# Kernel optimization log

Measured on AMD Instinct MI355X. Metric: run time of the kernel, lower is better.

Reference implementation:

```python
import jax, jax.numpy as jnp
import numpy as np

B, LAT, HID, N, H = 16, 128, 256, 256, 4
C = HID // H
TAU = 1.0


def setup_inputs() -> dict:
    key = jax.random.key(0)
    ks = jax.random.split(key, 16)
    g = lambda k, shape: (jax.random.normal(k, shape, dtype=jnp.float32) * 0.05)
    u = jax.random.uniform(ks[15], (B, N, N), dtype=jnp.float32, minval=1e-6, maxval=1.0 - 1e-6)
    gumbel = -jnp.log(-jnp.log(u))
    return {
        "x": jax.random.normal(ks[0], (B, LAT), dtype=jnp.float32),
        "W0": g(ks[1], (LAT, HID)), "b0": g(ks[2], (HID,)),
        "W1": g(ks[3], (HID, HID)), "b1": g(ks[4], (HID,)),
        "W2": g(ks[5], (HID, N * HID)), "b2": g(ks[6], (N * HID,)),
        "Wg": g(ks[7], (HID, H * C)),
        "att_src": g(ks[8], (H, C)), "att_dst": g(ks[9], (H, C)),
        "bg": g(ks[10], (H * C,)),
        "Wl": g(ks[11], (HID, N)), "bl": g(ks[12], (N,)),
        "gumbel": gumbel,
    }


def _forward(x, W0, b0, W1, b1, W2, b2, Wg, att_src, att_dst, bg, Wl, bl, gumbel):
    batch = x.shape[0]
    n = bl.shape[0]
    heads, ch = att_src.shape
    hid = heads * ch
    # MLP: latent -> hidden -> hidden -> n_nodes*hidden
    h = jax.nn.relu(x @ W0 + b0)
    h = jax.nn.relu(h @ W1 + b1)
    h = (h @ W2 + b2).reshape(batch, n, hid)
    # edge list: torch.combinations (i<j) directed src->dst, plus PyG self-loops
    s_np, d_np = np.triu_indices(n, k=1)
    src = jnp.concatenate([jnp.asarray(s_np, dtype=jnp.int32), jnp.arange(n, dtype=jnp.int32)])
    dst = jnp.concatenate([jnp.asarray(d_np, dtype=jnp.int32), jnp.arange(n, dtype=jnp.int32)])

    def gat(xn):  # xn: [N, hid]
        gfeat = (xn @ Wg).reshape(n, heads, ch)
        a_s = jnp.einsum('nhc,hc->nh', gfeat, att_src)
        a_d = jnp.einsum('nhc,hc->nh', gfeat, att_dst)
        e = jax.nn.leaky_relu(a_s[src] + a_d[dst], 0.2)          # [E, H]
        m = jax.lax.stop_gradient(jax.ops.segment_max(e, dst, num_segments=n))
        p = jnp.exp(e - m[dst])
        denom = jax.ops.segment_sum(p, dst, num_segments=n)
        alpha = p / denom[dst]                                   # segment softmax per dst
        out = jax.ops.segment_sum(gfeat[src] * alpha[:, :, None], dst, num_segments=n)
        return out.reshape(n, hid) + bg

    h = jax.nn.elu(jax.vmap(gat)(h))  # dropout is a no-op (eval mode)
    logits = h @ Wl + bl
    # gumbel_softmax(hard=True) with straight-through estimator
    y_soft = jax.nn.softmax((logits + gumbel) / TAU, axis=-1)
    y_hard = jax.nn.one_hot(jnp.argmax(y_soft, axis=-1), n, dtype=y_soft.dtype)
    y = jax.lax.stop_gradient(y_hard - y_soft) + y_soft
    adj = jnp.clip(y + jnp.swapaxes(y, 1, 2), 0.0, 1.0)
    return adj


def reference(x, W0, b0, W1, b1, W2, b2, Wg, att_src, att_dst, bg, Wl, bl, gumbel):
    return _forward(x, W0, b0, W1, b1, W2, b2, Wg, att_src, att_dst, bg, Wl, bl, gumbel)
```

## Files before the change

### kernel.cpp

```cpp
#include <hip/hip_runtime.h>
#include <hip/hip_bf16.h>
#include <math.h>

#define NB 16
#define LAT 128
#define HID 256
#define NN 256
#define NH 4
#define JT 8

__device__ __forceinline__ float lrelu02(float x){ return x > 0.f ? x : 0.2f*x; }
__device__ __forceinline__ float eluf(float x){ return x > 0.f ? x : expm1f(x); }

__global__ __launch_bounds__(256) void k_mlp12(const float* __restrict__ x,
    const float* __restrict__ W0, const float* __restrict__ b0,
    const float* __restrict__ W1, const float* __restrict__ b1,
    float* __restrict__ h2)
{
    __shared__ float xs[LAT];
    __shared__ float h1s[HID];
    int b = blockIdx.x, t = threadIdx.x;
    if (t < LAT) xs[t] = x[b*LAT + t];
    __syncthreads();
    float acc = b0[t];
    for (int k = 0; k < LAT; ++k) acc = fmaf(xs[k], W0[k*HID + t], acc);
    h1s[t] = fmaxf(acc, 0.f);
    __syncthreads();
    float acc2 = b1[t];
    for (int k = 0; k < HID; ++k) acc2 = fmaf(h1s[k], W1[k*HID + t], acc2);
    h2[b*HID + t] = fmaxf(acc2, 0.f);
}

__global__ __launch_bounds__(256) void k_mlp3g(
    const float* __restrict__ h2, const float* __restrict__ W2,
    const float* __restrict__ b2, const float* __restrict__ Wg,
    const float* __restrict__ att_src, const float* __restrict__ att_dst,
    float* __restrict__ gfeat, float* __restrict__ a_s, float* __restrict__ a_d)
{
    __shared__ float h2T[HID][16];
    __shared__ float h3s[NB][HID+1];
    int t = threadIdx.x;
    int n = blockIdx.x;
    for (int idx = t; idx < NB*HID; idx += 256) {
        int b = idx & 15, k = idx >> 4;
        h2T[k][b] = h2[b*HID + k];
    }
    __syncthreads();
    float acc[NB];
    #pragma unroll
    for (int b = 0; b < NB; ++b) acc[b] = 0.f;
    const float* w2p = W2 + (size_t)n*HID + t;
    for (int k0 = 0; k0 < HID; k0 += 8) {
        float wv[8];
        #pragma unroll
        for (int u = 0; u < 8; ++u) wv[u] = w2p[(size_t)(k0+u)*65536];
        #pragma unroll
        for (int u = 0; u < 8; ++u) {
            const float* hr = &h2T[k0+u][0];
            #pragma unroll
            for (int b = 0; b < NB; ++b) acc[b] = fmaf(hr[b], wv[u], acc[b]);
        }
    }
    float bv = b2[n*HID + t];
    #pragma unroll
    for (int b = 0; b < NB; ++b) h3s[b][t] = acc[b] + bv;
    __syncthreads();
    int l = t & 63, w = t >> 6, cb = l*4;
    float4 g[4];
    #pragma unroll
    for (int rr = 0; rr < 4; ++rr) g[rr] = make_float4(0.f,0.f,0.f,0.f);
    #pragma unroll 4
    for (int k = 0; k < HID; ++k) {
        float4 wg = *(const float4*)&Wg[k*HID + cb];
        #pragma unroll
        for (int rr = 0; rr < 4; ++rr) {
            float hv = h3s[w*4+rr][k];
            g[rr].x = fmaf(hv, wg.x, g[rr].x);
            g[rr].y = fmaf(hv, wg.y, g[rr].y);
            g[rr].z = fmaf(hv, wg.z, g[rr].z);
            g[rr].w = fmaf(hv, wg.w, g[rr].w);
        }
    }
    float4 s4 = *(const float4*)&att_src[cb];
    float4 d4 = *(const float4*)&att_dst[cb];
    int h = l >> 4;
    #pragma unroll
    for (int rr = 0; rr < 4; ++rr) {
        int b = w*4 + rr;
        *(float4*)&gfeat[b*(NN*HID) + n*HID + cb] = g[rr];
        float ps = g[rr].x*s4.x + g[rr].y*s4.y + g[rr].z*s4.z + g[rr].w*s4.w;
        float pd = g[rr].x*d4.x + g[rr].y*d4.y + g[rr].z*d4.z + g[rr].w*d4.w;
        #pragma unroll
        for (int off = 1; off < 16; off <<= 1) {
            ps += __shfl_xor(ps, off);
            pd += __shfl_xor(pd, off);
        }
        if ((l & 15) == 0) {
            a_s[b*(NN*NH) + n*NH + h] = ps;
            a_d[b*(NN*NH) + n*NH + h] = pd;
        }
    }
}

__global__ __launch_bounds__(64) void k_prefmax(const float* __restrict__ a_s,
    float* __restrict__ prefM)
{
    int bh = blockIdx.x; int b = bh >> 2, h = bh & 3;
    int l = threadIdx.x;
    float carry = -INFINITY;
    for (int ch = 0; ch < 4; ++ch) {
        int n = ch*64 + l;
        float v = a_s[b*(NN*NH) + n*NH + h];
        #pragma unroll
        for (int off = 1; off < 64; off <<= 1) {
            float u = __shfl_up(v, off);
            if (l >= off) v = fmaxf(v, u);
        }
        v = fmaxf(v, carry);
        prefM[b*(NN*NH) + n*NH + h] = v;
        carry = __shfl(v, 63);
    }
}

__global__ __launch_bounds__(256) void k_gatlog(
    const float* __restrict__ gfeat, const float* __restrict__ a_s,
    const float* __restrict__ a_d, const float* __restrict__ prefM,
    const float* __restrict__ bg, const float* __restrict__ Wl,
    const float* __restrict__ bl, const float* __restrict__ gumbel,
    int* __restrict__ biOut)
{
    __shared__ float pa[4*2052];
    __shared__ float part[4*JT*256];
    __shared__ float houtsT[NN][8];
    __shared__ float wsum[4][32];
    __shared__ float redv[4][JT];
    __shared__ int   redi[4][JT];

    int t = threadIdx.x;
    int bb = blockIdx.y;
    int j0 = blockIdx.x * JT;
    int l = t & 63, w = t >> 6;

    float4 as4 = *(const float4*)&a_s[bb*(NN*NH) + t*NH];
    float p[JT][4];
    #pragma unroll
    for (int jj = 0; jj < JT; ++jj) {
        int j = j0 + jj;
        float4 ad4 = *(const float4*)&a_d[bb*(NN*NH) + j*NH];
        float4 pm4 = *(const float4*)&prefM[bb*(NN*NH) + j*NH];
        bool valid = (t <= j);
        p[jj][0] = valid ? expf(lrelu02(as4.x+ad4.x) - lrelu02(pm4.x+ad4.x)) : 0.f;
        p[jj][1] = valid ? expf(lrelu02(as4.y+ad4.y) - lrelu02(pm4.y+ad4.y)) : 0.f;
        p[jj][2] = valid ? expf(lrelu02(as4.z+ad4.z) - lrelu02(pm4.z+ad4.z)) : 0.f;
        p[jj][3] = valid ? expf(lrelu02(as4.w+ad4.w) - lrelu02(pm4.w+ad4.w)) : 0.f;
    }
    #pragma unroll
    for (int jj = 0; jj < JT; ++jj)
        #pragma unroll
        for (int h = 0; h < 4; ++h) {
            float s = p[jj][h];
            #pragma unroll
            for (int off = 1; off < 64; off <<= 1) s += __shfl_xor(s, off);
            if (l == 0) wsum[w][jj*4+h] = s;
        }
    __syncthreads();
    #pragma unroll
    for (int jj = 0; jj < JT; ++jj)
        #pragma unroll
        for (int h = 0; h < 4; ++h) {
            int c = jj*4+h;
            float denom = wsum[0][c] + wsum[1][c] + wsum[2][c] + wsum[3][c];
            pa[h*2052 + t*8 + jj] = p[jj][h] / denom;
        }
    __syncthreads();

    int q = l >> 4, c4 = (l & 15)*4;
    float4 aj[JT];
    #pragma unroll
    for (int jj = 0; jj < JT; ++jj) aj[jj] = make_float4(0.f,0.f,0.f,0.f);
    const float* gb = gfeat + bb*(NN*HID);
    for (int ii = 0; ii < 64; ++ii) {
        int ig = w*64 + ii;
        float4 g4 = *(const float4*)&gb[ig*HID + q*64 + c4];
        float4 pv0 = *(const float4*)&pa[q*2052 + ig*8];
        float4 pv1 = *(const float4*)&pa[q*2052 + ig*8 + 4];
        aj[0].x = fmaf(pv0.x, g4.x, aj[0].x); aj[0].y = fmaf(pv0.x, g4.y, aj[0].y);
        aj[0].z = fmaf(pv0.x, g4.z, aj[0].z); aj[0].w = fmaf(pv0.x, g4.w, aj[0].w);
        aj[1].x = fmaf(pv0.y, g4.x, aj[1].x); aj[1].y = fmaf(pv0.y, g4.y, aj[1].y);
        aj[1].z = fmaf(pv0.y, g4.z, aj[1].z); aj[1].w = fmaf(pv0.y, g4.w, aj[1].w);
        aj[2].x = fmaf(pv0.z, g4.x, aj[2].x); aj[2].y = fmaf(pv0.z, g4.y, aj[2].y);
        aj[2].z = fmaf(pv0.z, g4.z, aj[2].z); aj[2].w = fmaf(pv0.z, g4.w, aj[2].w);
        aj[3].x = fmaf(pv0.w, g4.x, aj[3].x); aj[3].y = fmaf(pv0.w, g4.y, aj[3].y);
        aj[3].z = fmaf(pv0.w, g4.z, aj[3].z); aj[3].w = fmaf(pv0.w, g4.w, aj[3].w);
        aj[4].x = fmaf(pv1.x, g4.x, aj[4].x); aj[4].y = fmaf(pv1.x, g4.y, aj[4].y);
        aj[4].z = fmaf(pv1.x, g4.z, aj[4].z); aj[4].w = fmaf(pv1.x, g4.w, aj[4].w);
        aj[5].x = fmaf(pv1.y, g4.x, aj[5].x); aj[5].y = fmaf(pv1.y, g4.y, aj[5].y);
        aj[5].z = fmaf(pv1.y, g4.z, aj[5].z); aj[5].w = fmaf(pv1.y, g4.w, aj[5].w);
        aj[6].x = fmaf(pv1.z, g4.x, aj[6].x); aj[6].y = fmaf(pv1.z, g4.y, aj[6].y);
        aj[6].z = fmaf(pv1.z, g4.z, aj[6].z); aj[6].w = fmaf(pv1.z, g4.w, aj[6].w);
        aj[7].x = fmaf(pv1.w, g4.x, aj[7].x); aj[7].y = fmaf(pv1.w, g4.y, aj[7].y);
        aj[7].z = fmaf(pv1.w, g4.z, aj[7].z); aj[7].w = fmaf(pv1.w, g4.w, aj[7].w);
    }
    #pragma unroll
    for (int jj = 0; jj < JT; ++jj)
        *(float4*)&part[(w*JT + jj)*256 + q*64 + c4] = aj[jj];
    __syncthreads();

    {
        float bgv = bg[t];
        #pragma unroll
        for (int jj = 0; jj < JT; ++jj) {
            float s = part[(0*JT+jj)*256 + t] + part[(1*JT+jj)*256 + t]
                    + part[(2*JT+jj)*256 + t] + part[(3*JT+jj)*256 + t] + bgv;
            houtsT[t][jj] = eluf(s);
        }
    }
    __syncthreads();

    int cb = l*4;
    float4 lg[JT];
    #pragma unroll
    for (int jj = 0; jj < JT; ++jj) lg[jj] = make_float4(0.f,0.f,0.f,0.f);
    for (int kk = 0; kk < 64; ++kk) {
        int k = w*64 + kk;
        float4 hA = *(const float4*)&houtsT[k][0];
        float4 hB = *(const float4*)&houtsT[k][4];
        float4 wl4 = *(const float4*)&Wl[k*HID + cb];
        lg[0].x = fmaf(hA.x, wl4.x, lg[0].x); lg[0].y = fmaf(hA.x, wl4.y, lg[0].y);
        lg[0].z = fmaf(hA.x, wl4.z, lg[0].z); lg[0].w = fmaf(hA.x, wl4.w, lg[0].w);
        lg[1].x = fmaf(hA.y, wl4.x, lg[1].x); lg[1].y = fmaf(hA.y, wl4.y, lg[1].y);
        lg[1].z = fmaf(hA.y, wl4.z, lg[1].z); lg[1].w = fmaf(hA.y, wl4.w, lg[1].w);
        lg[2].x = fmaf(hA.z, wl4.x, lg[2].x); lg[2].y = fmaf(hA.z, wl4.y, lg[2].y);
        lg[2].z = fmaf(hA.z, wl4.z, lg[2].z); lg[2].w = fmaf(hA.z, wl4.w, lg[2].w);
        lg[3].x = fmaf(hA.w, wl4.x, lg[3].x); lg[3].y = fmaf(hA.w, wl4.y, lg[3].y);
        lg[3].z = fmaf(hA.w, wl4.z, lg[3].z); lg[3].w = fmaf(hA.w, wl4.w, lg[3].w);
        lg[4].x = fmaf(hB.x, wl4.x, lg[4].x); lg[4].y = fmaf(hB.x, wl4.y, lg[4].y);
        lg[4].z = fmaf(hB.x, wl4.z, lg[4].z); lg[4].w = fmaf(hB.x, wl4.w, lg[4].w);
        lg[5].x = fmaf(hB.y, wl4.x, lg[5].x); lg[5].y = fmaf(hB.y, wl4.y, lg[5].y);
        lg[5].z = fmaf(hB.y, wl4.z, lg[5].z); lg[5].w = fmaf(hB.y, wl4.w, lg[5].w);
        lg[6].x = fmaf(hB.z, wl4.x, lg[6].x); lg[6].y = fmaf(hB.z, wl4.y, lg[6].y);
        lg[6].z = fmaf(hB.z, wl4.z, lg[6].z); lg[6].w = fmaf(hB.z, wl4.w, lg[6].w);
        lg[7].x = fmaf(hB.w, wl4.x, lg[7].x); lg[7].y = fmaf(hB.w, wl4.y, lg[7].y);
        lg[7].z = fmaf(hB.w, wl4.z, lg[7].z); lg[7].w = fmaf(hB.w, wl4.w, lg[7].w);
    }
    __syncthreads();
    #pragma unroll
    for (int jj = 0; jj < JT; ++jj)
        *(float4*)&part[(w*JT + jj)*256 + cb] = lg[jj];
    __syncthreads();

    {
        float blv = bl[t];
        #pragma unroll
        for (int jj = 0; jj < JT; ++jj) {
            float z = part[(0*JT+jj)*256 + t] + part[(1*JT+jj)*256 + t]
                    + part[(2*JT+jj)*256 + t] + part[(3*JT+jj)*256 + t]
                    + blv + gumbel[bb*(NN*NN) + (j0+jj)*NN + t];
            float bv = z; int bi_ = t;
            #pragma unroll
            for (int off = 1; off < 64; off <<= 1) {
                float ov = __shfl_xor(bv, off);
                int   oi = __shfl_xor(bi_, off);
                if (ov > bv || (ov == bv && oi < bi_)) { bv = ov; bi_ = oi; }
            }
            if (l == 0) { redv[w][jj] = bv; redi[w][jj] = bi_; }
        }
    }
    __syncthreads();
    if (t < JT) {
        float bv = redv[0][t]; int bi_ = redi[0][t];
        #pragma unroll
        for (int ww = 1; ww < 4; ++ww)
            if (redv[ww][t] > bv) { bv = redv[ww][t]; bi_ = redi[ww][t]; }
        biOut[bb*NN + j0 + t] = bi_;
    }
}

__global__ __launch_bounds__(256) void k_adj(const int* __restrict__ bi,
    float* __restrict__ adj)
{
    int bb = blockIdx.x, t = threadIdx.x;
    float4* ap = (float4*)(adj + (size_t)bb*(NN*NN));
    float4 z = make_float4(0.f,0.f,0.f,0.f);
    for (int idx = t; idx < NN*NN/4; idx += 256) ap[idx] = z;
    __syncthreads();
    int b = bi[bb*NN + t];
    adj[(size_t)bb*(NN*NN) + t*NN + b] = 1.0f;
    adj[(size_t)bb*(NN*NN) + b*NN + t] = 1.0f;
}

extern "C" void kernel_launch(void* const* d_in, const int* in_sizes, int n_in,
                              void* d_out, int out_size, void* d_ws, size_t ws_size,
                              hipStream_t stream)
{
    const float* x       = (const float*)d_in[0];
    const float* W0      = (const float*)d_in[1];
    const float* b0      = (const float*)d_in[2];
    const float* W1      = (const float*)d_in[3];
    const float* b1      = (const float*)d_in[4];
    const float* W2      = (const float*)d_in[5];
    const float* b2      = (const float*)d_in[6];
    const float* Wg      = (const float*)d_in[7];
    const float* att_src = (const float*)d_in[8];
    const float* att_dst = (const float*)d_in[9];
    const float* bg      = (const float*)d_in[10];
    const float* Wl      = (const float*)d_in[11];
    const float* bl      = (const float*)d_in[12];
    const float* gumbel  = (const float*)d_in[13];

    float* ws    = (float*)d_ws;
    float* h2    = ws;
    float* a_s   = h2 + 4096;
    float* a_d   = a_s + 16384;
    float* prefM = a_d + 16384;
    int*   biIdx = (int*)(prefM + 16384);
    float* gfeat = (float*)d_out;
    float* adj   = (float*)d_out;

    k_mlp12 <<<NB, 256, 0, stream>>>(x, W0, b0, W1, b1, h2);
    k_mlp3g <<<NN, 256, 0, stream>>>(h2, W2, b2, Wg, att_src, att_dst, gfeat, a_s, a_d);
    k_prefmax<<<NB*NH, 64, 0, stream>>>(a_s, prefM);
    k_gatlog<<<dim3(NN/JT, NB), 256, 0, stream>>>(gfeat, a_s, a_d, prefM, bg, Wl, bl, gumbel, biIdx);
    k_adj   <<<NB, 256, 0, stream>>>(biIdx, adj);
}
```

Measured before the change: 103.8 us.

## Precompute softmax denominators, skip masked tiles, split-K the MLP, and remap blocks to XCDs

A new kernel computes each destination's full softmax normaliser, written as exp(-m)/sum, and replaces the prefix-max kernel. The GAT kernel can then skip its in-block reductions and bound the aggregation loop to the causal source range, so work on masked (i>j) rows is dropped. The MLP layer-3 kernel uses 512 threads and splits K in two with a shared-memory reduction. JT is halved, giving 1024 blocks, and the block index is remapped so each batch's blocks stay on the same XCD. The risks are the cost of the extra denominator pass and a softmax scaling whose numerics differ from the reference.

```diff
diff --git a/kernel.cpp b/kernel.cpp
--- a/kernel.cpp
+++ b/kernel.cpp
@@ -1,5 +1,4 @@
 #include <hip/hip_runtime.h>
-#include <hip/hip_bf16.h>
 #include <math.h>
 
 #define NB 16
@@ -7,7 +6,7 @@
 #define HID 256
 #define NN 256
 #define NH 4
-#define JT 8
+#define JT 4
 
 __device__ __forceinline__ float lrelu02(float x){ return x > 0.f ? x : 0.2f*x; }
 __device__ __forceinline__ float eluf(float x){ return x > 0.f ? x : expm1f(x); }
@@ -31,17 +30,19 @@
     h2[b*HID + t] = fmaxf(acc2, 0.f);
 }
 
-__global__ __launch_bounds__(256) void k_mlp3g(
+__global__ __launch_bounds__(512) void k_mlp3g(
     const float* __restrict__ h2, const float* __restrict__ W2,
     const float* __restrict__ b2, const float* __restrict__ Wg,
     const float* __restrict__ att_src, const float* __restrict__ att_dst,
     float* __restrict__ gfeat, float* __restrict__ a_s, float* __restrict__ a_d)
 {
     __shared__ float h2T[HID][16];
+    __shared__ float red[256*17];
     __shared__ float h3s[NB][HID+1];
     int t = threadIdx.x;
     int n = blockIdx.x;
-    for (int idx = t; idx < NB*HID; idx += 256) {
+    int col = t & 255, kh = t >> 8;
+    for (int idx = t; idx < NB*HID; idx += 512) {
         int b = idx & 15, k = idx >> 4;
         h2T[k][b] = h2[b*HID + k];
     }
@@ -49,32 +50,38 @@
     float acc[NB];
     #pragma unroll
     for (int b = 0; b < NB; ++b) acc[b] = 0.f;
-    const float* w2p = W2 + (size_t)n*HID + t;
-    for (int k0 = 0; k0 < HID; k0 += 8) {
-        float wv[8];
-        #pragma unroll
-        for (int u = 0; u < 8; ++u) wv[u] = w2p[(size_t)(k0+u)*65536];
-        #pragma unroll
-        for (int u = 0; u < 8; ++u) {
-            const float* hr = &h2T[k0+u][0];
+    const float* w2p = W2 + (size_t)kh*128*65536 + (size_t)n*HID + col;
+    for (int k0 = 0; k0 < 128; k0 += 16) {
+        float wv[16];
+        #pragma unroll
+        for (int u = 0; u < 16; ++u) wv[u] = w2p[(size_t)(k0+u)*65536];
+        #pragma unroll
+        for (int u = 0; u < 16; ++u) {
+            const float* hr = &h2T[kh*128 + k0 + u][0];
             #pragma unroll
             for (int b = 0; b < NB; ++b) acc[b] = fmaf(hr[b], wv[u], acc[b]);
         }
     }
-    float bv = b2[n*HID + t];
-    #pragma unroll
-    for (int b = 0; b < NB; ++b) h3s[b][t] = acc[b] + bv;
+    if (kh == 1) {
+        #pragma unroll
+        for (int b = 0; b < NB; ++b) red[col*17 + b] = acc[b];
+    }
+    __syncthreads();
+    if (kh == 0) {
+        float bv = b2[n*HID + col];
+        #pragma unroll
+        for (int b = 0; b < NB; ++b) h3s[b][col] = acc[b] + red[col*17 + b] + bv;
+    }
     __syncthreads();
     int l = t & 63, w = t >> 6, cb = l*4;
-    float4 g[4];
-    #pragma unroll
-    for (int rr = 0; rr < 4; ++rr) g[rr] = make_float4(0.f,0.f,0.f,0.f);
+    float4 g[2];
+    g[0] = make_float4(0.f,0.f,0.f,0.f); g[1] = g[0];
     #pragma unroll 4
     for (int k = 0; k < HID; ++k) {
         float4 wg = *(const float4*)&Wg[k*HID + cb];
         #pragma unroll
-        for (int rr = 0; rr < 4; ++rr) {
-            float hv = h3s[w*4+rr][k];
+        for (int rr = 0; rr < 2; ++rr) {
+            float hv = h3s[w*2+rr][k];
             g[rr].x = fmaf(hv, wg.x, g[rr].x);
             g[rr].y = fmaf(hv, wg.y, g[rr].y);
             g[rr].z = fmaf(hv, wg.z, g[rr].z);
@@ -85,8 +92,8 @@
     float4 d4 = *(const float4*)&att_dst[cb];
     int h = l >> 4;
     #pragma unroll
-    for (int rr = 0; rr < 4; ++rr) {
-        int b = w*4 + rr;
+    for (int rr = 0; rr < 2; ++rr) {
+        int b = w*2 + rr;
         *(float4*)&gfeat[b*(NN*HID) + n*HID + cb] = g[rr];
         float ps = g[rr].x*s4.x + g[rr].y*s4.y + g[rr].z*s4.z + g[rr].w*s4.w;
         float pd = g[rr].x*d4.x + g[rr].y*d4.y + g[rr].z*d4.z + g[rr].w*d4.w;
@@ -102,104 +109,96 @@
     }
 }
 
-__global__ __launch_bounds__(64) void k_prefmax(const float* __restrict__ a_s,
-    float* __restrict__ prefM)
-{
-    int bh = blockIdx.x; int b = bh >> 2, h = bh & 3;
-    int l = threadIdx.x;
-    float carry = -INFINITY;
-    for (int ch = 0; ch < 4; ++ch) {
-        int n = ch*64 + l;
-        float v = a_s[b*(NN*NH) + n*NH + h];
-        #pragma unroll
-        for (int off = 1; off < 64; off <<= 1) {
-            float u = __shfl_up(v, off);
-            if (l >= off) v = fmaxf(v, u);
-        }
-        v = fmaxf(v, carry);
-        prefM[b*(NN*NH) + n*NH + h] = v;
-        carry = __shfl(v, 63);
+__global__ __launch_bounds__(256) void k_prefden(const float* __restrict__ a_s,
+    const float* __restrict__ a_d, float* __restrict__ sArr)
+{
+    __shared__ float as_sh[NN];
+    int id = blockIdx.x;
+    int b = id >> 4, h = (id >> 2) & 3, jc = id & 3;
+    int t = threadIdx.x;
+    as_sh[t] = a_s[b*(NN*NH) + t*NH + h];
+    __syncthreads();
+    int jl = t >> 2, r = t & 3;
+    int j = jc*64 + jl;
+    float ad = a_d[b*(NN*NH) + j*NH + h];
+    float lm = -INFINITY;
+    for (int i = r; i <= j; i += 4) lm = fmaxf(lm, as_sh[i]);
+    lm = fmaxf(lm, __shfl_xor(lm, 1));
+    lm = fmaxf(lm, __shfl_xor(lm, 2));
+    float m = lrelu02(lm + ad);
+    float s = 0.f;
+    for (int i = r; i <= j; i += 4) s += expf(lrelu02(as_sh[i] + ad) - m);
+    s += __shfl_xor(s, 1);
+    s += __shfl_xor(s, 2);
+    if (r == 0) {
+        sArr[b*(NN*NH) + j*NH + h] = expf(-m) / s;
     }
 }
 
 __global__ __launch_bounds__(256) void k_gatlog(
     const float* __restrict__ gfeat, const float* __restrict__ a_s,
-    const float* __restrict__ a_d, const float* __restrict__ prefM,
+    const float* __restrict__ a_d, const float* __restrict__ sArr,
     const float* __restrict__ bg, const float* __restrict__ Wl,
     const float* __restrict__ bl, const float* __restrict__ gumbel,
     int* __restrict__ biOut)
 {
-    __shared__ float pa[4*2052];
-    __shared__ float part[4*JT*256];
-    __shared__ float houtsT[NN][8];
-    __shared__ float wsum[4][32];
+    __shared__ float pa[4*1032];
+    __shared__ float part[16*256];
+    __shared__ float houts[NN*4];
     __shared__ float redv[4][JT];
     __shared__ int   redi[4][JT];
 
     int t = threadIdx.x;
-    int bb = blockIdx.y;
-    int j0 = blockIdx.x * JT;
+    int id = blockIdx.x;
+    int xcd = id & 7, k2 = id >> 3;
+    int bb = (xcd << 1) | (k2 >> 6);
+    int j0 = (k2 & 63) * JT;
     int l = t & 63, w = t >> 6;
 
-    float4 as4 = *(const float4*)&a_s[bb*(NN*NH) + t*NH];
-    float p[JT][4];
-    #pragma unroll
-    for (int jj = 0; jj < JT; ++jj) {
-        int j = j0 + jj;
-        float4 ad4 = *(const float4*)&a_d[bb*(NN*NH) + j*NH];
-        float4 pm4 = *(const float4*)&prefM[bb*(NN*NH) + j*NH];
-        bool valid = (t <= j);
-        p[jj][0] = valid ? expf(lrelu02(as4.x+ad4.x) - lrelu02(pm4.x+ad4.x)) : 0.f;
-        p[jj][1] = valid ? expf(lrelu02(as4.y+ad4.y) - lrelu02(pm4.y+ad4.y)) : 0.f;
-        p[jj][2] = valid ? expf(lrelu02(as4.z+ad4.z) - lrelu02(pm4.z+ad4.z)) : 0.f;
-        p[jj][3] = valid ? expf(lrelu02(as4.w+ad4.w) - lrelu02(pm4.w+ad4.w)) : 0.f;
-    }
-    #pragma unroll
-    for (int jj = 0; jj < JT; ++jj)
-        #pragma unroll
-        for (int h = 0; h < 4; ++h) {
-            float s = p[jj][h];
+    float pr[JT][4];
+    if (w*64 <= j0 + JT - 1) {
+        float4 as4 = *(const float4*)&a_s[bb*(NN*NH) + t*NH];
+        #pragma unroll
+        for (int jj = 0; jj < JT; ++jj) {
+            int j = j0 + jj;
+            float4 ad4 = *(const float4*)&a_d[bb*(NN*NH) + j*NH];
+            float4 sv4 = *(const float4*)&sArr[bb*(NN*NH) + j*NH];
+            bool valid = (t <= j);
+            pr[jj][0] = valid ? expf(lrelu02(as4.x+ad4.x)) * sv4.x : 0.f;
+            pr[jj][1] = valid ? expf(lrelu02(as4.y+ad4.y)) * sv4.y : 0.f;
+            pr[jj][2] = valid ? expf(lrelu02(as4.z+ad4.z)) * sv4.z : 0.f;
+            pr[jj][3] = valid ? expf(lrelu02(as4.w+ad4.w)) * sv4.w : 0.f;
+        }
+    } else {
+        #pragma unroll
+        for (int jj = 0; jj < JT; ++jj)
             #pragma unroll
-            for (int off = 1; off < 64; off <<= 1) s += __shfl_xor(s, off);
-            if (l == 0) wsum[w][jj*4+h] = s;
-        }
-    __syncthreads();
-    #pragma unroll
-    for (int jj = 0; jj < JT; ++jj)
-        #pragma unroll
-        for (int h = 0; h < 4; ++h) {
-            int c = jj*4+h;
-            float denom = wsum[0][c] + wsum[1][c] + wsum[2][c] + wsum[3][c];
-            pa[h*2052 + t*8 + jj] = p[jj][h] / denom;
-        }
-    __syncthreads();
-
-    int q = l >> 4, c4 = (l & 15)*4;
+            for (int h = 0; h < 4; ++h) pr[jj][h] = 0.f;
+    }
+    #pragma unroll
+    for (int h = 0; h < 4; ++h)
+        *(float4*)&pa[h*1032 + t*4] = make_float4(pr[0][h], pr[1][h], pr[2][h], pr[3][h]);
+    __syncthreads();
+
+    int q = l >> 4, c4 = (l & 15) * 4;
     float4 aj[JT];
     #pragma unroll
     for (int jj = 0; jj < JT; ++jj) aj[jj] = make_float4(0.f,0.f,0.f,0.f);
     const float* gb = gfeat + bb*(NN*HID);
-    for (int ii = 0; ii < 64; ++ii) {
+    int lim = j0 + JT - w*64; lim = lim < 0 ? 0 : (lim > 64 ? 64 : lim);
+    #pragma unroll 4
+    for (int ii = 0; ii < lim; ++ii) {
         int ig = w*64 + ii;
         float4 g4 = *(const float4*)&gb[ig*HID + q*64 + c4];
-        float4 pv0 = *(const float4*)&pa[q*2052 + ig*8];
-        float4 pv1 = *(const float4*)&pa[q*2052 + ig*8 + 4];
-        aj[0].x = fmaf(pv0.x, g4.x, aj[0].x); aj[0].y = fmaf(pv0.x, g4.y, aj[0].y);
-        aj[0].z = fmaf(pv0.x, g4.z, aj[0].z); aj[0].w = fmaf(pv0.x, g4.w, aj[0].w);
-        aj[1].x = fmaf(pv0.y, g4.x, aj[1].x); aj[1].y = fmaf(pv0.y, g4.y, aj[1].y);
-        aj[1].z = fmaf(pv0.y, g4.z, aj[1].z); aj[1].w = fmaf(pv0.y, g4.w, aj[1].w);
-        aj[2].x = fmaf(pv0.z, g4.x, aj[2].x); aj[2].y = fmaf(pv0.z, g4.y, aj[2].y);
-        aj[2].z = fmaf(pv0.z, g4.z, aj[2].z); aj[2].w = fmaf(pv0.z, g4.w, aj[2].w);
-        aj[3].x = fmaf(pv0.w, g4.x, aj[3].x); aj[3].y = fmaf(pv0.w, g4.y, aj[3].y);
-        aj[3].z = fmaf(pv0.w, g4.z, aj[3].z); aj[3].w = fmaf(pv0.w, g4.w, aj[3].w);
-        aj[4].x = fmaf(pv1.x, g4.x, aj[4].x); aj[4].y = fmaf(pv1.x, g4.y, aj[4].y);
-        aj[4].z = fmaf(pv1.x, g4.z, aj[4].z); aj[4].w = fmaf(pv1.x, g4.w, aj[4].w);
-        aj[5].x = fmaf(pv1.y, g4.x, aj[5].x); aj[5].y = fmaf(pv1.y, g4.y, aj[5].y);
-        aj[5].z = fmaf(pv1.y, g4.z, aj[5].z); aj[5].w = fmaf(pv1.y, g4.w, aj[5].w);
-        aj[6].x = fmaf(pv1.z, g4.x, aj[6].x); aj[6].y = fmaf(pv1.z, g4.y, aj[6].y);
-        aj[6].z = fmaf(pv1.z, g4.z, aj[6].z); aj[6].w = fmaf(pv1.z, g4.w, aj[6].w);
-        aj[7].x = fmaf(pv1.w, g4.x, aj[7].x); aj[7].y = fmaf(pv1.w, g4.y, aj[7].y);
-        aj[7].z = fmaf(pv1.w, g4.z, aj[7].z); aj[7].w = fmaf(pv1.w, g4.w, aj[7].w);
+        float4 pv = *(const float4*)&pa[q*1032 + ig*4];
+        aj[0].x = fmaf(pv.x, g4.x, aj[0].x); aj[0].y = fmaf(pv.x, g4.y, aj[0].y);
+        aj[0].z = fmaf(pv.x, g4.z, aj[0].z); aj[0].w = fmaf(pv.x, g4.w, aj[0].w);
+        aj[1].x = fmaf(pv.y, g4.x, aj[1].x); aj[1].y = fmaf(pv.y, g4.y, aj[1].y);
+        aj[1].z = fmaf(pv.y, g4.z, aj[1].z); aj[1].w = fmaf(pv.y, g4.w, aj[1].w);
+        aj[2].x = fmaf(pv.z, g4.x, aj[2].x); aj[2].y = fmaf(pv.z, g4.y, aj[2].y);
+        aj[2].z = fmaf(pv.z, g4.z, aj[2].z); aj[2].w = fmaf(pv.z, g4.w, aj[2].w);
+        aj[3].x = fmaf(pv.w, g4.x, aj[3].x); aj[3].y = fmaf(pv.w, g4.y, aj[3].y);
+        aj[3].z = fmaf(pv.w, g4.z, aj[3].z); aj[3].w = fmaf(pv.w, g4.w, aj[3].w);
     }
     #pragma unroll
     for (int jj = 0; jj < JT; ++jj)
@@ -208,12 +207,14 @@
 
     {
         float bgv = bg[t];
+        float hh[JT];
         #pragma unroll
         for (int jj = 0; jj < JT; ++jj) {
             float s = part[(0*JT+jj)*256 + t] + part[(1*JT+jj)*256 + t]
                     + part[(2*JT+jj)*256 + t] + part[(3*JT+jj)*256 + t] + bgv;
-            houtsT[t][jj] = eluf(s);
-        }
+            hh[jj] = eluf(s);
+        }
+        *(float4*)&houts[t*4] = make_float4(hh[0], hh[1], hh[2], hh[3]);
     }
     __syncthreads();
 
@@ -221,50 +222,39 @@
     float4 lg[JT];
     #pragma unroll
     for (int jj = 0; jj < JT; ++jj) lg[jj] = make_float4(0.f,0.f,0.f,0.f);
+    #pragma unroll 2
     for (int kk = 0; kk < 64; ++kk) {
         int k = w*64 + kk;
-        float4 hA = *(const float4*)&houtsT[k][0];
-        float4 hB = *(const float4*)&houtsT[k][4];
+        float4 hv  = *(const float4*)&houts[k*4];
         float4 wl4 = *(const float4*)&Wl[k*HID + cb];
-        lg[0].x = fmaf(hA.x, wl4.x, lg[0].x); lg[0].y = fmaf(hA.x, wl4.y, lg[0].y);
-        lg[0].z = fmaf(hA.x, wl4.z, lg[0].z); lg[0].w = fmaf(hA.x, wl4.w, lg[0].w);
-        lg[1].x = fmaf(hA.y, wl4.x, lg[1].x); lg[1].y = fmaf(hA.y, wl4.y, lg[1].y);
-        lg[1].z = fmaf(hA.y, wl4.z, lg[1].z); lg[1].w = fmaf(hA.y, wl4.w, lg[1].w);
-        lg[2].x = fmaf(hA.z, wl4.x, lg[2].x); lg[2].y = fmaf(hA.z, wl4.y, lg[2].y);
-        lg[2].z = fmaf(hA.z, wl4.z, lg[2].z); lg[2].w = fmaf(hA.z, wl4.w, lg[2].w);
-        lg[3].x = fmaf(hA.w, wl4.x, lg[3].x); lg[3].y = fmaf(hA.w, wl4.y, lg[3].y);
-        lg[3].z = fmaf(hA.w, wl4.z, lg[3].z); lg[3].w = fmaf(hA.w, wl4.w, lg[3].w);
-        lg[4].x = fmaf(hB.x, wl4.x, lg[4].x); lg[4].y = fmaf(hB.x, wl4.y, lg[4].y);
-        lg[4].z = fmaf(hB.x, wl4.z, lg[4].z); lg[4].w = fmaf(hB.x, wl4.w, lg[4].w);
-        lg[5].x = fmaf(hB.y, wl4.x, lg[5].x); lg[5].y = fmaf(hB.y, wl4.y, lg[5].y);
-        lg[5].z = fmaf(hB.y, wl4.z, lg[5].z); lg[5].w = fmaf(hB.y, wl4.w, lg[5].w);
-        lg[6].x = fmaf(hB.z, wl4.x, lg[6].x); lg[6].y = fmaf(hB.z, wl4.y, lg[6].y);
-        lg[6].z = fmaf(hB.z, wl4.z, lg[6].z); lg[6].w = fmaf(hB.z, wl4.w, lg[6].w);
-        lg[7].x = fmaf(hB.w, wl4.x, lg[7].x); lg[7].y = fmaf(hB.w, wl4.y, lg[7].y);
-        lg[7].z = fmaf(hB.w, wl4.z, lg[7].z); lg[7].w = fmaf(hB.w, wl4.w, lg[7].w);
-    }
-    __syncthreads();
+        lg[0].x = fmaf(hv.x, wl4.x, lg[0].x); lg[0].y = fmaf(hv.x, wl4.y, lg[0].y);
+        lg[0].z = fmaf(hv.x, wl4.z, lg[0].z); lg[0].w = fmaf(hv.x, wl4.w, lg[0].w);
+        lg[1].x = fmaf(hv.y, wl4.x, lg[1].x); lg[1].y = fmaf(hv.y, wl4.y, lg[1].y);
+        lg[1].z = fmaf(hv.y, wl4.z, lg[1].z); lg[1].w = fmaf(hv.y, wl4.w, lg[1].w);
+        lg[2].x = fmaf(hv.z, wl4.x, lg[2].x); lg[2].y = fmaf(hv.z, wl4.y, lg[2].y);
+        lg[2].z = fmaf(hv.z, wl4.z, lg[2].z); lg[2].w = fmaf(hv.z, wl4.w, lg[2].w);
+        lg[3].x = fmaf(hv.w, wl4.x, lg[3].x); lg[3].y = fmaf(hv.w, wl4.y, lg[3].y);
+        lg[3].z = fmaf(hv.w, wl4.z, lg[3].z); lg[3].w = fmaf(hv.w, wl4.w, lg[3].w);
+    }
     #pragma unroll
     for (int jj = 0; jj < JT; ++jj)
         *(float4*)&part[(w*JT + jj)*256 + cb] = lg[jj];
     __syncthreads();
 
-    {
-        float blv = bl[t];
-        #pragma unroll
-        for (int jj = 0; jj < JT; ++jj) {
-            float z = part[(0*JT+jj)*256 + t] + part[(1*JT+jj)*256 + t]
-                    + part[(2*JT+jj)*256 + t] + part[(3*JT+jj)*256 + t]
-                    + blv + gumbel[bb*(NN*NN) + (j0+jj)*NN + t];
-            float bv = z; int bi_ = t;
-            #pragma unroll
-            for (int off = 1; off < 64; off <<= 1) {
-                float ov = __shfl_xor(bv, off);
-                int   oi = __shfl_xor(bi_, off);
-                if (ov > bv || (ov == bv && oi < bi_)) { bv = ov; bi_ = oi; }
-            }
-            if (l == 0) { redv[w][jj] = bv; redi[w][jj] = bi_; }
-        }
+    float blv = bl[t];
+    #pragma unroll
+    for (int jj = 0; jj < JT; ++jj) {
+        float z = part[(0*JT+jj)*256 + t] + part[(1*JT+jj)*256 + t]
+                + part[(2*JT+jj)*256 + t] + part[(3*JT+jj)*256 + t]
+                + blv + gumbel[bb*(NN*NN) + (j0+jj)*NN + t];
+        float bv = z; int bi_ = t;
+        #pragma unroll
+        for (int off = 1; off < 64; off <<= 1) {
+            float ov = __shfl_xor(bv, off);
+            int   oi = __shfl_xor(bi_, off);
+            if (ov > bv || (ov == bv && oi < bi_)) { bv = ov; bi_ = oi; }
+        }
+        if (l == 0) { redv[w][jj] = bv; redi[w][jj] = bi_; }
     }
     __syncthreads();
     if (t < JT) {
@@ -308,18 +298,18 @@
     const float* bl      = (const float*)d_in[12];
     const float* gumbel  = (const float*)d_in[13];
 
-    float* ws    = (float*)d_ws;
-    float* h2    = ws;
-    float* a_s   = h2 + 4096;
-    float* a_d   = a_s + 16384;
-    float* prefM = a_d + 16384;
-    int*   biIdx = (int*)(prefM + 16384);
-    float* gfeat = (float*)d_out;
-    float* adj   = (float*)d_out;
-
-    k_mlp12 <<<NB, 256, 0, stream>>>(x, W0, b0, W1, b1, h2);
-    k_mlp3g <<<NN, 256, 0, stream>>>(h2, W2, b2, Wg, att_src, att_dst, gfeat, a_s, a_d);
-    k_prefmax<<<NB*NH, 64, 0, stream>>>(a_s, prefM);
-    k_gatlog<<<dim3(NN/JT, NB), 256, 0, stream>>>(gfeat, a_s, a_d, prefM, bg, Wl, bl, gumbel, biIdx);
-    k_adj   <<<NB, 256, 0, stream>>>(biIdx, adj);
-}
+    float* ws     = (float*)d_ws;
+    float* h2     = ws;
+    float* a_s    = h2 + 4096;
+    float* a_d    = a_s + 16384;
+    float* sArr   = a_d + 16384;
+    int*   biIdx  = (int*)(sArr + 16384);
+    float* gfeat  = (float*)d_out;
+    float* adj    = (float*)d_out;
+
+    k_mlp12  <<<NB, 256, 0, stream>>>(x, W0, b0, W1, b1, h2);
+    k_mlp3g  <<<NN, 512, 0, stream>>>(h2, W2, b2, Wg, att_src, att_dst, gfeat, a_s, a_d);
+    k_prefden<<<256, 256, 0, stream>>>(a_s, a_d, sArr);
+    k_gatlog <<<NB*64, 256, 0, stream>>>(gfeat, a_s, a_d, sArr, bg, Wl, bl, gumbel, biIdx);
+    k_adj    <<<NB, 256, 0, stream>>>(biIdx, adj);
+}
```

Result: faster. 88.86 us, median of 2 (-14.4%).
